# Kernel optimization log

Measured on AMD Instinct MI355X. Metric: run time of the kernel, lower is better.

## Reference

```python
import jax, jax.numpy as jnp
import numpy as np

B, N, E = 4, 20000, 320000
DA, DB, H, OUT = 64, 64, 128, 1  # feature dims, hidden_dim, output_dim; DA+DB == H


def setup_inputs() -> dict:
    key = jax.random.key(0)
    ks = jax.random.split(key, 9)
    feat_a = jax.random.normal(ks[0], (B, N, DA), dtype=jnp.float32)
    feat_b = jax.random.normal(ks[1], (B, N, DB), dtype=jnp.float32)
    edge_index = jax.random.randint(ks[2], (2, E), 0, N)
    s = 1.0 / np.sqrt(H)
    W_gcn = jax.random.normal(ks[3], (H, H), dtype=jnp.float32) * s
    b_gcn = jnp.zeros((H,), dtype=jnp.float32)
    W1 = jax.random.normal(ks[4], (H, H), dtype=jnp.float32) * s
    b1 = jax.random.normal(ks[5], (H,), dtype=jnp.float32) * 0.01
    W2 = jax.random.normal(ks[6], (H, OUT), dtype=jnp.float32) * s
    b2 = jnp.zeros((OUT,), dtype=jnp.float32)
    return {"feat_a": feat_a, "feat_b": feat_b, "edge_index": edge_index,
            "W_gcn": W_gcn, "b_gcn": b_gcn, "W1": W1, "b1": b1, "W2": W2, "b2": b2}


def _gcn_conv(x, src, dst, W, b):
    # x: [B, N, H_in]; GCNConv: out = D^-1/2 (A+I) D^-1/2 (x W) + b
    n = x.shape[1]
    loops = jnp.arange(n)
    src_sl = jnp.concatenate([src, loops])  # add self-loops
    dst_sl = jnp.concatenate([dst, loops])
    deg = jax.ops.segment_sum(jnp.ones_like(src_sl, dtype=x.dtype), dst_sl, num_segments=n)
    dinv = jnp.where(deg > 0, jax.lax.rsqrt(deg), 0.0)
    norm = dinv[src_sl] * dinv[dst_sl]  # [E+N]
    h = x @ W  # [B, N, H]

    def agg(hb):  # hb: [N, H]
        msgs = hb[src_sl] * norm[:, None]  # gather + scale, [E+N, H]
        return jax.ops.segment_sum(msgs, dst_sl, num_segments=n)  # scatter-add

    return jax.vmap(agg)(h) + b


def reference(feat_a, feat_b, edge_index, W_gcn, b_gcn, W1, b1, W2, b2):
    combined = jnp.concatenate([feat_a, feat_b], axis=-1)  # [B, N, H]
    gcn_out = _gcn_conv(combined, edge_index[0], edge_index[1], W_gcn, b_gcn)
    pooled = gcn_out.mean(axis=1)  # mean over nodes -> [B, H]
    hid = jax.nn.relu(pooled @ W1 + b1)  # dropout is identity in eval
    logits = hid @ W2 + b2  # [B, 1]
    return logits
```

## Files before the change

kernel.cpp:

```cpp
#include <hip/hip_runtime.h>

#define NB 4
#define NN 20000
#define NE 320000
#define HH 128

#define EBLK 64
#define HTHR 1024
#define CHUNKS 256
#define WTHR 512
#define PER 79
#define NSEC 8

#define RB 79

#define OFF_PDEG 0
#define OFF_DINV (EBLK * NN)
#define OFF_PS   (OFF_DINV + NN)
#define OFF_V    (OFF_PS + EBLK * NN)
#define OFF_CNT  (OFF_V + NSEC * NB * HH)

__global__ void __launch_bounds__(HTHR) deg_hist_kernel(
        const int* __restrict__ dst, float* __restrict__ pdeg) {
    __shared__ float hist[NN];
    const int t = threadIdx.x, bk = blockIdx.x;
    for (int i = t; i < NN; i += HTHR) hist[i] = 0.0f;
    __syncthreads();
    for (int e = bk * HTHR + t; e < NE; e += EBLK * HTHR)
        atomicAdd(&hist[dst[e]], 1.0f);
    __syncthreads();
    float* out = pdeg + (size_t)bk * NN;
    for (int i = t; i < NN; i += HTHR) out[i] = hist[i];
}

__global__ void reduce_deg_kernel(const float* __restrict__ pdeg,
                                  float* __restrict__ dinv,
                                  float* __restrict__ v, int* __restrict__ cnts) {
    if (blockIdx.x == 0) {
        #pragma unroll
        for (int u = 0; u < NSEC * NB * HH / 256; ++u)
            v[u * 256 + threadIdx.x] = 0.0f;
        if (threadIdx.x < 9) cnts[threadIdx.x] = 0;
    }
    const int n = blockIdx.x * 256 + threadIdx.x;
    if (n >= NN) return;
    float acc = 1.0f;
    #pragma unroll 8
    for (int c = 0; c < EBLK; ++c) acc += pdeg[(size_t)c * NN + n];
    dinv[n] = rsqrtf(acc);
}

__global__ void __launch_bounds__(HTHR) s_hist_kernel(
        const int* __restrict__ src, const int* __restrict__ dst,
        const float* __restrict__ dinv, float* __restrict__ ps) {
    __shared__ float hist[NN];
    const int t = threadIdx.x, bk = blockIdx.x;
    for (int i = t; i < NN; i += HTHR) hist[i] = 0.0f;
    __syncthreads();
    for (int e = bk * HTHR + t; e < NE; e += EBLK * HTHR)
        atomicAdd(&hist[src[e]], dinv[dst[e]]);
    __syncthreads();
    float* out = ps + (size_t)bk * NN;
    for (int i = t; i < NN; i += HTHR) out[i] = hist[i];
}

__global__ void __launch_bounds__(WTHR) wsum_mlp_kernel(
        const float* __restrict__ fa, const float* __restrict__ fb,
        const float* __restrict__ dinv, const float* __restrict__ ps,
        const float* __restrict__ Wg, const float* __restrict__ bg,
        const float* __restrict__ W1, const float* __restrict__ b1,
        const float* __restrict__ W2, const float* __restrict__ b2,
        float* __restrict__ v, int* __restrict__ cnts,
        float* __restrict__ out) {
    __shared__ float WL[HH * HH];
    __shared__ float xs[NB * HH];
    __shared__ float ys[NB * HH];
    __shared__ float red[NB * HH];
    __shared__ float wl[PER];
    __shared__ float wpart[PER][8];
    __shared__ float4 smem[WTHR];
    int* sub = cnts;
    int* master = cnts + 8;
    const int t = threadIdx.x;

    if (blockIdx.x == 0) {
        const float4* wgv = (const float4*)Wg;
        const float4* w1v = (const float4*)W1;
        float4* wlv = (float4*)WL;
        float warm = 0.0f;
        for (int i = t; i < HH * HH / 4; i += WTHR) {
            wlv[i] = wgv[i];
            float4 y = w1v[i];
            warm += y.x + y.w;
        }
        asm volatile("" :: "v"(warm));
        if (t == 0) {
            while (atomicAdd(master, 0) < NSEC) __builtin_amdgcn_s_sleep(8);
        }
        __syncthreads();

        float val = 0.0f;
        #pragma unroll
        for (int s = 0; s < NSEC; ++s)
            val += atomicAdd(&v[s * (NB * HH) + t], 0.0f);
        xs[t] = val * (1.0f / NN);
        __syncthreads();

        const int bb = t >> 7;
        const int kk = t & (HH - 1);

        float a1 = bg[kk];
        #pragma unroll 8
        for (int j = 0; j < HH; ++j) a1 += xs[bb * HH + j] * WL[j * HH + kk];
        ys[t] = a1;
        __syncthreads();

        for (int i = t; i < HH * HH / 4; i += WTHR) wlv[i] = w1v[i];
        __syncthreads();
        float a2 = b1[kk];
        #pragma unroll 8
        for (int j = 0; j < HH; ++j) a2 += ys[bb * HH + j] * WL[j * HH + kk];
        a2 = fmaxf(a2, 0.0f);
        red[t] = a2 * W2[kk];
        __syncthreads();

        #pragma unroll
        for (int off = HH / 2; off > 0; off >>= 1) {
            if (kk < off) red[bb * HH + kk] += red[bb * HH + kk + off];
            __syncthreads();
        }
        if (kk == 0) out[bb] = red[bb * HH] + b2[0];
        return;
    }

    const int c = blockIdx.x - 1;
    const int n0 = c * PER;
    const int n1 = min(NN, n0 + PER);
    const int cnt = n1 - n0;
    float* vsec = v + (size_t)(c & (NSEC - 1)) * (NB * HH);

    if (cnt > 0) {
        for (int idx = t; idx < cnt * 8; idx += WTHR) {
            const int i = idx >> 3, s = idx & 7;
            const int n = n0 + i;
            float a = 0.0f;
            #pragma unroll
            for (int u = 0; u < 8; ++u) a += ps[(size_t)(s * 8 + u) * NN + n];
            wpart[i][s] = a;
        }
        __syncthreads();
        for (int i = t; i < cnt; i += WTHR) {
            float a = 0.0f;
            #pragma unroll
            for (int s = 0; s < 8; ++s) a += wpart[i][s];
            const float di = dinv[n0 + i];
            wl[i] = di * (di + a);
        }
        __syncthreads();

        const int g = t >> 5;
        const int q = t & 31;
        const float* base = (q < 16) ? (fa + (size_t)q * 4)
                                     : (fb + (size_t)(q - 16) * 4);

        float4 acc[NB];
        #pragma unroll
        for (int b = 0; b < NB; ++b) acc[b] = make_float4(0.f, 0.f, 0.f, 0.f);

        int n = n0 + g;
        for (; n + 48 < n1; n += 64) {
            const float w0 = wl[n - n0];
            const float w1 = wl[n + 16 - n0];
            const float w2 = wl[n + 32 - n0];
            const float w3 = wl[n + 48 - n0];
            #pragma unroll
            for (int b = 0; b < NB; ++b) {
                const float* p = base + ((size_t)b * NN + n) * 64;
                float4 x0 = *reinterpret_cast<const float4*>(p);
                float4 x1 = *reinterpret_cast<const float4*>(p + 16 * 64);
                float4 x2 = *reinterpret_cast<const float4*>(p + 32 * 64);
                float4 x3 = *reinterpret_cast<const float4*>(p + 48 * 64);
                acc[b].x += w0 * x0.x + w1 * x1.x + w2 * x2.x + w3 * x3.x;
                acc[b].y += w0 * x0.y + w1 * x1.y + w2 * x2.y + w3 * x3.y;
                acc[b].z += w0 * x0.z + w1 * x1.z + w2 * x2.z + w3 * x3.z;
                acc[b].w += w0 * x0.w + w1 * x1.w + w2 * x2.w + w3 * x3.w;
            }
        }
        for (; n < n1; n += 16) {
            const float wn = wl[n - n0];
            #pragma unroll
            for (int b = 0; b < NB; ++b) {
                float4 x = *reinterpret_cast<const float4*>(
                    base + ((size_t)b * NN + n) * 64);
                acc[b].x += wn * x.x; acc[b].y += wn * x.y;
                acc[b].z += wn * x.z; acc[b].w += wn * x.w;
            }
        }

        #pragma unroll
        for (int b = 0; b < NB; ++b) {
            smem[t] = acc[b];
            __syncthreads();
            if (t < 32) {
                float4 r = smem[t];
                #pragma unroll
                for (int gg = 1; gg < 16; ++gg) {
                    float4 o = smem[gg * 32 + t];
                    r.x += o.x; r.y += o.y; r.z += o.z; r.w += o.w;
                }
                const int k = (t < 16) ? t * 4 : 64 + (t - 16) * 4;
                float* vb = vsec + b * HH + k;
                atomicAdd(vb + 0, r.x);
                atomicAdd(vb + 1, r.y);
                atomicAdd(vb + 2, r.z);
                atomicAdd(vb + 3, r.w);
            }
            __syncthreads();
        }
    }

    if (t == 0) {
        asm volatile("s_waitcnt vmcnt(0)" ::: "memory");
        int old = atomicAdd(&sub[c & (NSEC - 1)], 1);
        if (old == (CHUNKS / NSEC) - 1) atomicAdd(master, 1);
    }
}

extern "C" void kernel_launch(void* const* d_in, const int* in_sizes, int n_in,
                              void* d_out, int out_size, void* d_ws, size_t ws_size,
                              hipStream_t stream) {
    const float* fa = (const float*)d_in[0];
    const float* fb = (const float*)d_in[1];
    const int*   ei = (const int*)d_in[2];
    const float* Wg = (const float*)d_in[3];
    const float* bg = (const float*)d_in[4];
    const float* W1 = (const float*)d_in[5];
    const float* b1 = (const float*)d_in[6];
    const float* W2 = (const float*)d_in[7];
    const float* b2 = (const float*)d_in[8];
    float* out = (float*)d_out;

    const int* src = ei;
    const int* dst = ei + NE;

    float* ws   = (float*)d_ws;
    float* pdeg = ws + OFF_PDEG;
    float* dinv = ws + OFF_DINV;
    float* ps   = ws + OFF_PS;
    float* v    = ws + OFF_V;
    int*   cnts = (int*)(ws + OFF_CNT);

    deg_hist_kernel<<<EBLK, HTHR, 0, stream>>>(dst, pdeg);

    reduce_deg_kernel<<<RB, 256, 0, stream>>>(pdeg, dinv, v, cnts);

    s_hist_kernel<<<EBLK, HTHR, 0, stream>>>(src, dst, dinv, ps);

    wsum_mlp_kernel<<<CHUNKS + 1, WTHR, 0, stream>>>(fa, fb, dinv, ps,
                                                     Wg, bg, W1, b1, W2, b2,
                                                     v, cnts, out);
}
```

Measured before the change: 51.13 us.

## Double weighted-sum chunks, vectorize histogram init/copy, drop shared weight staging in MLP

```diff
diff --git a/kernel.cpp b/kernel.cpp
--- a/kernel.cpp
+++ b/kernel.cpp
@@ -7,10 +7,10 @@
 
 #define EBLK 64
 #define HTHR 1024
-#define CHUNKS 256
+#define CHUNKS 512
 #define WTHR 512
-#define PER 79
-#define NSEC 8
+#define PER 40
+#define NSEC 16
 
 #define RB 79
 
@@ -22,15 +22,17 @@
 
 __global__ void __launch_bounds__(HTHR) deg_hist_kernel(
         const int* __restrict__ dst, float* __restrict__ pdeg) {
-    __shared__ float hist[NN];
+    __shared__ __align__(16) float hist[NN];
     const int t = threadIdx.x, bk = blockIdx.x;
-    for (int i = t; i < NN; i += HTHR) hist[i] = 0.0f;
+    float4* h4 = (float4*)hist;
+    const float4 z4 = make_float4(0.f, 0.f, 0.f, 0.f);
+    for (int i = t; i < NN / 4; i += HTHR) h4[i] = z4;
     __syncthreads();
     for (int e = bk * HTHR + t; e < NE; e += EBLK * HTHR)
         atomicAdd(&hist[dst[e]], 1.0f);
     __syncthreads();
-    float* out = pdeg + (size_t)bk * NN;
-    for (int i = t; i < NN; i += HTHR) out[i] = hist[i];
+    float4* out = (float4*)(pdeg + (size_t)bk * NN);
+    for (int i = t; i < NN / 4; i += HTHR) out[i] = h4[i];
 }
 
 __global__ void reduce_deg_kernel(const float* __restrict__ pdeg,
@@ -40,7 +42,7 @@
         #pragma unroll
         for (int u = 0; u < NSEC * NB * HH / 256; ++u)
             v[u * 256 + threadIdx.x] = 0.0f;
-        if (threadIdx.x < 9) cnts[threadIdx.x] = 0;
+        if (threadIdx.x < 17) cnts[threadIdx.x] = 0;
     }
     const int n = blockIdx.x * 256 + threadIdx.x;
     if (n >= NN) return;
@@ -53,15 +55,17 @@
 __global__ void __launch_bounds__(HTHR) s_hist_kernel(
         const int* __restrict__ src, const int* __restrict__ dst,
         const float* __restrict__ dinv, float* __restrict__ ps) {
-    __shared__ float hist[NN];
+    __shared__ __align__(16) float hist[NN];
     const int t = threadIdx.x, bk = blockIdx.x;
-    for (int i = t; i < NN; i += HTHR) hist[i] = 0.0f;
+    float4* h4 = (float4*)hist;
+    const float4 z4 = make_float4(0.f, 0.f, 0.f, 0.f);
+    for (int i = t; i < NN / 4; i += HTHR) h4[i] = z4;
     __syncthreads();
     for (int e = bk * HTHR + t; e < NE; e += EBLK * HTHR)
         atomicAdd(&hist[src[e]], dinv[dst[e]]);
     __syncthreads();
-    float* out = ps + (size_t)bk * NN;
-    for (int i = t; i < NN; i += HTHR) out[i] = hist[i];
+    float4* out = (float4*)(ps + (size_t)bk * NN);
+    for (int i = t; i < NN / 4; i += HTHR) out[i] = h4[i];
 }
 
 __global__ void __launch_bounds__(WTHR) wsum_mlp_kernel(
@@ -72,7 +76,6 @@
         const float* __restrict__ W2, const float* __restrict__ b2,
         float* __restrict__ v, int* __restrict__ cnts,
         float* __restrict__ out) {
-    __shared__ float WL[HH * HH];
     __shared__ float xs[NB * HH];
     __shared__ float ys[NB * HH];
     __shared__ float red[NB * HH];
@@ -80,22 +83,19 @@
     __shared__ float wpart[PER][8];
     __shared__ float4 smem[WTHR];
     int* sub = cnts;
-    int* master = cnts + 8;
+    int* master = cnts + 16;
     const int t = threadIdx.x;
 
     if (blockIdx.x == 0) {
-        const float4* wgv = (const float4*)Wg;
-        const float4* w1v = (const float4*)W1;
-        float4* wlv = (float4*)WL;
         float warm = 0.0f;
         for (int i = t; i < HH * HH / 4; i += WTHR) {
-            wlv[i] = wgv[i];
-            float4 y = w1v[i];
-            warm += y.x + y.w;
+            float4 a = ((const float4*)Wg)[i];
+            float4 b = ((const float4*)W1)[i];
+            warm += a.x + a.w + b.x + b.w;
         }
         asm volatile("" :: "v"(warm));
         if (t == 0) {
-            while (atomicAdd(master, 0) < NSEC) __builtin_amdgcn_s_sleep(8);
+            while (atomicAdd(master, 0) < NSEC) __builtin_amdgcn_s_sleep(16);
         }
         __syncthreads();
 
@@ -111,15 +111,13 @@
 
         float a1 = bg[kk];
         #pragma unroll 8
-        for (int j = 0; j < HH; ++j) a1 += xs[bb * HH + j] * WL[j * HH + kk];
+        for (int j = 0; j < HH; ++j) a1 += xs[bb * HH + j] * Wg[j * HH + kk];
         ys[t] = a1;
         __syncthreads();
 
-        for (int i = t; i < HH * HH / 4; i += WTHR) wlv[i] = w1v[i];
-        __syncthreads();
         float a2 = b1[kk];
         #pragma unroll 8
-        for (int j = 0; j < HH; ++j) a2 += ys[bb * HH + j] * WL[j * HH + kk];
+        for (int j = 0; j < HH; ++j) a2 += ys[bb * HH + j] * W1[j * HH + kk];
         a2 = fmaxf(a2, 0.0f);
         red[t] = a2 * W2[kk];
         __syncthreads();
@@ -167,26 +165,7 @@
         #pragma unroll
         for (int b = 0; b < NB; ++b) acc[b] = make_float4(0.f, 0.f, 0.f, 0.f);
 
-        int n = n0 + g;
-        for (; n + 48 < n1; n += 64) {
-            const float w0 = wl[n - n0];
-            const float w1 = wl[n + 16 - n0];
-            const float w2 = wl[n + 32 - n0];
-            const float w3 = wl[n + 48 - n0];
-            #pragma unroll
-            for (int b = 0; b < NB; ++b) {
-                const float* p = base + ((size_t)b * NN + n) * 64;
-                float4 x0 = *reinterpret_cast<const float4*>(p);
-                float4 x1 = *reinterpret_cast<const float4*>(p + 16 * 64);
-                float4 x2 = *reinterpret_cast<const float4*>(p + 32 * 64);
-                float4 x3 = *reinterpret_cast<const float4*>(p + 48 * 64);
-                acc[b].x += w0 * x0.x + w1 * x1.x + w2 * x2.x + w3 * x3.x;
-                acc[b].y += w0 * x0.y + w1 * x1.y + w2 * x2.y + w3 * x3.y;
-                acc[b].z += w0 * x0.z + w1 * x1.z + w2 * x2.z + w3 * x3.z;
-                acc[b].w += w0 * x0.w + w1 * x1.w + w2 * x2.w + w3 * x3.w;
-            }
-        }
-        for (; n < n1; n += 16) {
+        for (int n = n0 + g; n < n1; n += 16) {
             const float wn = wl[n - n0];
             #pragma unroll
             for (int b = 0; b < NB; ++b) {
```

Result: slower. 56.89 us (+11.3%).
